# Kernel tuning notes

Measured on AMD Instinct MI355X. Metric: run time of the kernel, lower is better.

## Reference

```python
import jax, jax.numpy as jnp
import numpy as np

B, D, O = 8192, 192, 16  # batch, input_dim==grid_size, output_dim


def setup_inputs() -> dict:
    key = jax.random.key(0)
    k1, k2 = jax.random.split(key)
    x = jax.random.uniform(k1, (B, D), dtype=jnp.float32)          # [B, D]
    splines = jax.random.normal(k2, (O, D, D), dtype=jnp.float32) * 0.05  # [O, grid, in]
    grid = jnp.linspace(0.0, 1.0, D, dtype=jnp.float32)            # [G] == [D]
    return {"x": x, "splines": splines, "grid": grid}


def reference(x, splines, grid):
    # Hat basis: basis[n, g, d] = relu(1 - |x[n, d] - grid[g]|)
    basis = jnp.maximum(0.0, 1.0 - jnp.abs(x[:, None, :] - grid[None, :, None]))  # [B, G, D]
    # out[n, i] = sum_{g, d} splines[i, g, d] * basis[n, g, d]
    return jnp.einsum("bgd,ogd->bo", basis, splines)  # [B, O]
```

## Files before the change

### kernel.cpp

```cpp
#include <hip/hip_runtime.h>
#include <hip/hip_bf16.h>


#define Dn 192
#define Gn 192
#define On 16
#define Bn 8192

#define DSPLIT 8
#define DCHUNK (Dn / DSPLIT)

__device__ __forceinline__ unsigned short f2bf(float f) {
    union { float f; unsigned u; } v; v.f = f;
    unsigned r = v.u + 0x7FFF + ((v.u >> 16) & 1);
    return (unsigned short)(r >> 16);
}

__global__ __launch_bounds__(256) void kan_pre(const float* __restrict__ sp,
                                               const float* __restrict__ grid,
                                               unsigned* __restrict__ tab,
                                               float* __restrict__ out) {
    int gtid = blockIdx.x * blockDim.x + threadIdx.x;
    if (gtid < Bn * On / 4)
        ((float4*)out)[gtid] = make_float4(0.f, 0.f, 0.f, 0.f);

    int w = gtid >> 6;
    int lane = threadIdx.x & 63;
    int dp = w >> 4;
    int i  = w & 15;
    int d  = dp * 2;

    int g0 = lane * 3;
    const float* s_base = sp + (size_t)i * Gn * Dn + d;
    float2 s0 = *(const float2*)&s_base[(size_t)(g0 + 0) * Dn];
    float2 s1 = *(const float2*)&s_base[(size_t)(g0 + 1) * Dn];
    float2 s2 = *(const float2*)&s_base[(size_t)(g0 + 2) * Dn];
    float r0 = grid[g0 + 0], r1 = grid[g0 + 1], r2 = grid[g0 + 2];

    #pragma unroll
    for (int j = 0; j < 2; ++j) {
        float v0 = (j == 0) ? s0.x : s0.y;
        float v1 = (j == 0) ? s1.x : s1.y;
        float v2 = (j == 0) ? s2.x : s2.y;
        float q0 = v0 * r0, q1 = v1 * r1, q2 = v2 * r2;

        float lp1 = v0 + v1, lp2 = lp1 + v2;
        float lq1 = q0 + q1, lq2 = lq1 + q2;
        float sP = lp2, sQ = lq2;
        #pragma unroll
        for (int off = 1; off < 64; off <<= 1) {
            float pP = __shfl_up(sP, off);
            float pQ = __shfl_up(sQ, off);
            if (lane >= off) { sP += pP; sQ += pQ; }
        }
        float exP = sP - lp2, exQ = sQ - lq2;
        float T = __shfl(sP, 63);
        float U = __shfl(sQ, 63);

        float P[3] = { exP + v0, exP + lp1, exP + lp2 };
        float Q[3] = { exQ + q0, exQ + lq1, exQ + lq2 };

        #pragma unroll
        for (int k = 0; k < 3; ++k) {
            int g = g0 + k;
            float A  = 2.0f * P[k] - T;
            float Cp = T - U + 2.0f * Q[k];
            tab[((size_t)(d + j) * Gn + g) * On + i] =
                (unsigned)f2bf(A) | ((unsigned)f2bf(Cp) << 16);
        }
    }
}

__global__ __launch_bounds__(256) void kan_main(const float* __restrict__ x,
                                                const unsigned* __restrict__ tab,
                                                float* __restrict__ out) {
    int t = threadIdx.x;
    int i  = t & 15;
    int nn = t >> 4;
    unsigned bid = blockIdx.x;
    int chunk = bid & 7;
    int n = (bid >> 3) * 16 + nn;
    int d0 = chunk * DCHUNK;

    const float4* xr = (const float4*)(x + (size_t)n * Dn + d0);
    const unsigned* tb = tab + (size_t)d0 * Gn * On + i;

    float acc = 0.0f;
    #pragma unroll
    for (int d4 = 0; d4 < DCHUNK / 4; ++d4) {
        float4 xv = xr[d4];
        float vx[4] = { xv.x, xv.y, xv.z, xv.w };
        #pragma unroll
        for (int k = 0; k < 4; ++k) {
            float v = vx[k];
            int g = (int)(v * 191.0f);
            g = (g < 0) ? 0 : (g > 191 ? 191 : g);
            unsigned e = __builtin_nontemporal_load(&tb[((d4 * 4 + k) * Gn + g) * On]);
            union { unsigned u; float f; } A, C;
            A.u = e << 16;
            C.u = e & 0xFFFF0000u;
            acc += C.f;
            acc = fmaf(-v, A.f, acc);
        }
    }
    atomicAdd(&out[(size_t)n * On + i], acc);
}

__global__ __launch_bounds__(256) void kan_naive(const float* __restrict__ x,
                                                 const float* __restrict__ sp,
                                                 const float* __restrict__ grid,
                                                 float* __restrict__ out) {
    __shared__ float xs[Dn];
    __shared__ float gsh[Gn];
    __shared__ float red[4];
    int n = blockIdx.x;
    int t = threadIdx.x;
    if (t < Dn) { xs[t] = x[(size_t)n * Dn + t]; gsh[t] = grid[t]; }
    __syncthreads();
    float acc[On];
    #pragma unroll
    for (int i = 0; i < On; ++i) acc[i] = 0.0f;
    for (int idx = t; idx < Gn * Dn; idx += 256) {
        int g = idx / Dn;
        int d = idx - g * Dn;
        float b = fmaxf(0.0f, 1.0f - fabsf(xs[d] - gsh[g]));
        #pragma unroll
        for (int i = 0; i < On; ++i)
            acc[i] += sp[(size_t)i * Gn * Dn + idx] * b;
    }
    for (int i = 0; i < On; ++i) {
        float v = acc[i];
        #pragma unroll
        for (int off = 32; off > 0; off >>= 1) v += __shfl_down(v, off);
        if ((t & 63) == 0) red[t >> 6] = v;
        __syncthreads();
        if (t == 0) out[(size_t)n * On + i] = red[0] + red[1] + red[2] + red[3];
        __syncthreads();
    }
}

extern "C" void kernel_launch(void* const* d_in, const int* in_sizes, int n_in,
                              void* d_out, int out_size, void* d_ws, size_t ws_size,
                              hipStream_t stream) {
    const float* x    = (const float*)d_in[0];
    const float* sp   = (const float*)d_in[1];
    const float* grid = (const float*)d_in[2];
    float* out = (float*)d_out;

    const size_t TAB_BYTES = (size_t)Dn * Gn * On * sizeof(unsigned);
    if (ws_size >= TAB_BYTES) {
        unsigned* tab = (unsigned*)d_ws;
        kan_pre<<<384, 256, 0, stream>>>(sp, grid, tab, out);
        kan_main<<<(Bn / 16) * DSPLIT, 256, 0, stream>>>(x, tab, out);
    } else {
        kan_naive<<<Bn, 256, 0, stream>>>(x, sp, grid, out);
    }
}
```

Baseline: 23.38 us.

## Stage x tiles in LDS and process eight rows per thread in kan_main

kan_main now uses 512-thread blocks covering 256 rows per D-chunk. Each block stages its x slice into shared memory with coalesced float4 loads, and each thread accumulates eight rows with their table gathers batched up front. This should raise memory-level parallelism for the table lookups and cut block count and launch overhead. The trade-offs are fewer blocks (256), which may underfill the GPU, and dropping the nontemporal load hint. The per-thread dd loop also reads LDS with a stride of 24 floats, which risks bank conflicts.

```diff
diff --git a/kernel.cpp b/kernel.cpp
--- a/kernel.cpp
+++ b/kernel.cpp
@@ -9,6 +9,8 @@
 
 #define DSPLIT 8
 #define DCHUNK (Dn / DSPLIT)
+#define NPBm 256
+#define TPBm 512
 
 __device__ __forceinline__ unsigned short f2bf(float f) {
     union { float f; unsigned u; } v; v.f = f;
@@ -71,39 +73,57 @@
     }
 }
 
-__global__ __launch_bounds__(256) void kan_main(const float* __restrict__ x,
-                                                const unsigned* __restrict__ tab,
-                                                float* __restrict__ out) {
+__global__ __launch_bounds__(TPBm) void kan_main(const float* __restrict__ x,
+                                                 const unsigned* __restrict__ tab,
+                                                 float* __restrict__ out) {
+    __shared__ float xs[NPBm * DCHUNK];
     int t = threadIdx.x;
-    int i  = t & 15;
-    int nn = t >> 4;
     unsigned bid = blockIdx.x;
     int chunk = bid & 7;
-    int n = (bid >> 3) * 16 + nn;
+    int n0 = (int)(bid >> 3) * NPBm;
     int d0 = chunk * DCHUNK;
 
-    const float4* xr = (const float4*)(x + (size_t)n * Dn + d0);
+    {
+        const float4* xsrc = (const float4*)x;
+        float4* xd = (float4*)xs;
+        #pragma unroll
+        for (int j = 0; j < (NPBm * DCHUNK / 4) / TPBm; ++j) {
+            int idx = t + j * TPBm;
+            int r = idx / 6, c = idx % 6;
+            xd[idx] = xsrc[(size_t)(n0 + r) * 48 + chunk * 6 + c];
+        }
+    }
+    __syncthreads();
+
+    int i    = t & 15;
+    int nsub = t >> 4;
     const unsigned* tb = tab + (size_t)d0 * Gn * On + i;
 
-    float acc = 0.0f;
-    #pragma unroll
-    for (int d4 = 0; d4 < DCHUNK / 4; ++d4) {
-        float4 xv = xr[d4];
-        float vx[4] = { xv.x, xv.y, xv.z, xv.w };
+    float acc[8] = {0.f, 0.f, 0.f, 0.f, 0.f, 0.f, 0.f, 0.f};
+    for (int dd = 0; dd < DCHUNK; ++dd) {
+        const unsigned* tbd = tb + (size_t)dd * Gn * On;
+        float v[8];
+        unsigned e[8];
         #pragma unroll
-        for (int k = 0; k < 4; ++k) {
-            float v = vx[k];
-            int g = (int)(v * 191.0f);
+        for (int k = 0; k < 8; ++k) {
+            float vv = xs[(nsub + 32 * k) * DCHUNK + dd];
+            int g = (int)(vv * 191.0f);
             g = (g < 0) ? 0 : (g > 191 ? 191 : g);
-            unsigned e = __builtin_nontemporal_load(&tb[((d4 * 4 + k) * Gn + g) * On]);
+            v[k] = vv;
+            e[k] = tbd[(size_t)g * On];
+        }
+        #pragma unroll
+        for (int k = 0; k < 8; ++k) {
             union { unsigned u; float f; } A, C;
-            A.u = e << 16;
-            C.u = e & 0xFFFF0000u;
-            acc += C.f;
-            acc = fmaf(-v, A.f, acc);
+            A.u = e[k] << 16;
+            C.u = e[k] & 0xFFFF0000u;
+            acc[k] += C.f;
+            acc[k] = fmaf(-v[k], A.f, acc[k]);
         }
     }
-    atomicAdd(&out[(size_t)n * On + i], acc);
+    #pragma unroll
+    for (int k = 0; k < 8; ++k)
+        atomicAdd(&out[(size_t)(n0 + nsub + 32 * k) * On + i], acc[k]);
 }
 
 __global__ __launch_bounds__(256) void kan_naive(const float* __restrict__ x,
@@ -151,7 +171,7 @@
     if (ws_size >= TAB_BYTES) {
         unsigned* tab = (unsigned*)d_ws;
         kan_pre<<<384, 256, 0, stream>>>(sp, grid, tab, out);
-        kan_main<<<(Bn / 16) * DSPLIT, 256, 0, stream>>>(x, tab, out);
+        kan_main<<<(Bn / NPBm) * DSPLIT, TPBm, 0, stream>>>(x, tab, out);
     } else {
         kan_naive<<<Bn, 256, 0, stream>>>(x, sp, grid, out);
     }
```

After: 28.08 us. 20.1% more time.
